# Kernel tuning notes

Measured on AMD Instinct MI355X. Metric: run time of the kernel, lower is better.

Reference implementation:

```python
import jax, jax.numpy as jnp
import numpy as np

B, S, F_IN, H, P2 = 64, 64, 2048, 512, 20  # batch, seq_len, input_size, hidden, 2*num_prototype


def setup_inputs() -> dict:
    key = jax.random.key(0)
    ks = jax.random.split(key, 16)
    sc = 0.02
    inp = {
        "v_feat": jax.random.normal(ks[0], (B, S, F_IN), jnp.float32),
        "category": jax.random.randint(ks[1], (B,), 0, 3, jnp.int64),
        "W_enc": jax.random.normal(ks[2], (F_IN, H), jnp.float32) * sc,
        "b_enc": jnp.zeros((H,), jnp.float32),
        # gate order along last axis: input, forget, output, memory(g)
        "Wx": jax.random.normal(ks[3], (H, 4 * H), jnp.float32) * sc,
        "bx": jnp.zeros((4 * H,), jnp.float32),
        "Wh": jax.random.normal(ks[4], (H, 4 * H), jnp.float32) * sc,
        "bh": jnp.zeros((4 * H,), jnp.float32),
        "cat_emb": jax.random.normal(ks[5], (3, H), jnp.float32) * sc,
        "W_dec": jax.random.normal(ks[6], (H, 1), jnp.float32) * sc,
        "b_dec": jnp.zeros((1,), jnp.float32),
        "prototype": jax.random.uniform(ks[7], (P2, F_IN), jnp.float32),
        "W_dd": jax.random.normal(ks[8], (P2 * S, 1), jnp.float32) * sc,
        "b_dd": jnp.zeros((1,), jnp.float32),
        "W_gate": jax.random.normal(ks[9], (F_IN, 1), jnp.float32) * sc,
        "b_gate": jnp.zeros((1,), jnp.float32),
    }
    return inp


def _forward(v_feat, category, W_enc, b_enc, Wx, bx, Wh, bh, cat_emb,
             W_dec, b_dec, prototype, W_dd, b_dd, W_gate, b_gate):
    batch, seq, feat = v_feat.shape
    # encoder + category fusion
    fuse = jax.nn.relu(jnp.einsum('bsf,fh->bsh', v_feat, W_enc) + b_enc)
    fuse = fuse + cat_emb[category][:, None, :]

    # fused-gate LSTM over time (note: original cell has NO tanh on cell in h = o*c)
    x_gates = jnp.einsum('bsh,hg->sbg', fuse, Wx) + (bx + bh)  # precompute input GEMM

    def step(carry, xg):
        h, c = carry
        gates = xg + h @ Wh
        i, f, o, g = jnp.split(gates, 4, axis=-1)
        i, f, o = jax.nn.sigmoid(i), jax.nn.sigmoid(f), jax.nn.sigmoid(o)
        g = jnp.tanh(g)
        c = f * c + i * g
        h = o * c
        return (h, c), None

    h0 = jnp.zeros((batch, Wh.shape[0]), fuse.dtype)
    (h, c), _ = jax.lax.scan(step, (h0, h0), x_gates)

    # dropout p=0.5 omitted (deterministic eval reference)
    output = jax.nn.sigmoid(h @ W_dec + b_dec)  # [B,1]

    # prototype distances: [B,S,2P]
    diff = v_feat[:, :, None, :] - prototype[None, None, :, :]
    dist = jnp.sum(diff * diff, axis=-1)
    dist_feat = jnp.log((dist + 1.0) / (dist + 1e-8))
    dist_pred = jax.nn.sigmoid(dist_feat.reshape(batch, -1) @ W_dd + b_dd)
    gate = jax.nn.sigmoid(jnp.mean(v_feat, axis=1) @ W_gate + b_gate)
    return output * gate + dist_pred * (1.0 - gate)


def reference(v_feat, category, W_enc, b_enc, Wx, bx, Wh, bh, cat_emb,
              W_dec, b_dec, prototype, W_dd, b_dd, W_gate, b_gate):
    return _forward(v_feat, category, W_enc, b_enc, Wx, bx, Wh, bh, cat_emb,
                    W_dec, b_dec, prototype, W_dd, b_dd, W_gate, b_gate)
```

## Files before the change

### kernel.cpp

```cpp
#include <hip/hip_runtime.h>
#include <cstdint>
#include <cstddef>


typedef __attribute__((ext_vector_type(8))) short short8;
typedef __attribute__((ext_vector_type(4))) float f32x4;
typedef unsigned long long ull;

__device__ __forceinline__ ushort f2bf(float x) {
    uint32_t u = __float_as_uint(x);
    return (ushort)((u + 0x7FFF + ((u >> 16) & 1)) >> 16);
}
__device__ __forceinline__ float bf2f(ushort u) {
    return __uint_as_float(((uint32_t)u) << 16);
}
__device__ __forceinline__ float sigm(float x) { return 1.f / (1.f + expf(-x)); }
__device__ __forceinline__ float tanh_fast(float x) { return 2.f / (1.f + expf(-2.f * x)) - 1.f; }

__global__ __launch_bounds__(256) void k_prep(
    const float* __restrict__ v_feat, const float* __restrict__ proto,
    const float* __restrict__ bx, const float* __restrict__ bh,
    const float* __restrict__ W_enc, const float* __restrict__ Wx,
    const float* __restrict__ Wh, const float* __restrict__ W_gate,
    ushort* __restrict__ v_bf16, ushort* __restrict__ proto_bf,
    float* __restrict__ bxh, ushort* __restrict__ Wenc_t,
    ushort* __restrict__ Wx_t, ushort* __restrict__ Whr,
    float* __restrict__ n2, float* __restrict__ gpart, float* __restrict__ p2,
    ushort* __restrict__ hbuf, int* __restrict__ flags, int* __restrict__ dd_done)
{
    __shared__ float ts[32][33];
    const int blk = blockIdx.x;
    const int tid = threadIdx.x;

    if (blk < 8192) {
        int i = blk * 256 + tid;
        float4 v = ((const float4*)v_feat)[i];
        ushort4 o;
        o.x = f2bf(v.x); o.y = f2bf(v.y); o.z = f2bf(v.z); o.w = f2bf(v.w);
        ((ushort4*)v_bf16)[i] = o;
    } else if (blk < 8232) {
        int i = (blk - 8192) * 256 + tid;
        float4 v = ((const float4*)proto)[i];
        ushort4 o;
        o.x = f2bf(v.x); o.y = f2bf(v.y); o.z = f2bf(v.z); o.w = f2bf(v.w);
        ((ushort4*)proto_bf)[i] = o;
    } else if (blk < 8244) {
        int row = 20 + (blk - 8232);
        ushort4 z = {0, 0, 0, 0};
        ((ushort4*)(proto_bf + (size_t)row * 2048))[tid * 2] = z;
        ((ushort4*)(proto_bf + (size_t)row * 2048))[tid * 2 + 1] = z;
    } else if (blk < 8252) {
        int n = (blk - 8244) * 256 + tid;
        int np = ((n & 511) << 2) | (n >> 9);
        bxh[np] = bx[n] + bh[n];
    } else if (blk < 11324) {
        const float* in;
        ushort* outp;
        int R, C, remap, t;
        if (blk < 9276)       { in = W_enc; outp = Wenc_t; R = 2048; C = 512;  remap = 0; t = blk - 8252; }
        else if (blk < 10300) { in = Wx;    outp = Wx_t;   R = 512;  C = 2048; remap = 1; t = blk - 9276; }
        else                  { in = Wh;    outp = Whr;    R = 512;  C = 2048; remap = 1; t = blk - 10300; }
        int tpr = C / 32;
        int cx = t % tpr, cy = t / tpr;
        int r0 = cy * 32, c0 = cx * 32;
        int rr = tid >> 3, cc = (tid & 7) * 4;
        float4 v = *(const float4*)(in + (size_t)(r0 + rr) * C + c0 + cc);
        ts[rr][cc + 0] = v.x; ts[rr][cc + 1] = v.y; ts[rr][cc + 2] = v.z; ts[rr][cc + 3] = v.w;
        __syncthreads();
        ushort4 o;
        o.x = f2bf(ts[cc + 0][rr]);
        o.y = f2bf(ts[cc + 1][rr]);
        o.z = f2bf(ts[cc + 2][rr]);
        o.w = f2bf(ts[cc + 3][rr]);
        int n = c0 + rr;
        int np = remap ? (((n & 511) << 2) | (n >> 9)) : n;
        *(ushort4*)(outp + (size_t)np * R + r0 + cc) = o;
    } else if (blk < 12348) {
        const int lane = tid & 63, w = tid >> 6;
        const int bs = (blk - 11324) * 4 + w;
        const float* vr = v_feat + (size_t)bs * 2048;
        float a = 0.f, g = 0.f;
#pragma unroll
        for (int i = 0; i < 8; ++i) {
            float4 x = ((const float4*)vr)[i * 64 + lane];
            float4 wg = ((const float4*)W_gate)[i * 64 + lane];
            a += x.x * x.x + x.y * x.y + x.z * x.z + x.w * x.w;
            g += x.x * wg.x + x.y * wg.y + x.z * wg.z + x.w * wg.w;
        }
#pragma unroll
        for (int o = 32; o > 0; o >>= 1) { a += __shfl_down(a, o); g += __shfl_down(g, o); }
        if (lane == 0) {
            n2[bs] = a;
            gpart[bs] = g;
        }
    } else if (blk == 12348) {
        const int lane = tid & 63, w = tid >> 6;
        for (int p = w; p < 20; p += 4) {
            const float* pr = proto + (size_t)p * 2048;
            float a = 0.f;
#pragma unroll
            for (int i = 0; i < 8; ++i) {
                float4 x = ((const float4*)pr)[i * 64 + lane];
                a += x.x * x.x + x.y * x.y + x.z * x.z + x.w * x.w;
            }
#pragma unroll
            for (int o = 32; o > 0; o >>= 1) a += __shfl_down(a, o);
            if (lane == 0) p2[p] = a;
        }
        if (tid == 0) *dd_done = 0;
    } else if (blk < 12381) {
        ((ull*)hbuf)[(blk - 12349) * 256 + tid] = 0ULL;
    } else {
        for (int i = tid; i < 2048; i += 256) flags[i] = 0;
    }
}

__global__ __launch_bounds__(256) void k_mid(
    const ushort* __restrict__ A, const ushort* __restrict__ Bt,
    const float* __restrict__ bias0,
    const float* __restrict__ cat_emb, const int* __restrict__ category,
    ushort* __restrict__ C,
    const ushort* __restrict__ proto_bf, float* __restrict__ dots)
{
    __shared__ ushort As[64][40];
    __shared__ ushort Bs[128][40];
    const int tid = threadIdx.x;
    const int lane = tid & 63, w = tid >> 6;
    const int quad = lane >> 4, l16 = lane & 15;
    const int blk = blockIdx.x;

    if (blk >= 256) {
        const int r0 = (blk - 256) * 64 + w * 16;
        f32x4 acc[2] = {};
        const ushort* arow = A + (size_t)(r0 + l16) * 2048 + quad * 8;
        const ushort* b0p = proto_bf + (size_t)l16 * 2048 + quad * 8;
        const ushort* b1p = proto_bf + (size_t)(16 + l16) * 2048 + quad * 8;
#pragma unroll 8
        for (int kk = 0; kk < 64; ++kk) {
            short8 af = *(const short8*)(arow + kk * 32);
            short8 bf0 = *(const short8*)(b0p + kk * 32);
            short8 bf1 = *(const short8*)(b1p + kk * 32);
            acc[0] = __builtin_amdgcn_mfma_f32_16x16x32_bf16(af, bf0, acc[0], 0, 0, 0);
            acc[1] = __builtin_amdgcn_mfma_f32_16x16x32_bf16(af, bf1, acc[1], 0, 0, 0);
        }
#pragma unroll
        for (int t = 0; t < 2; ++t)
#pragma unroll
            for (int r = 0; r < 4; ++r)
                dots[(size_t)(r0 + quad * 4 + r) * 32 + t * 16 + l16] = acc[t][r];
        return;
    }

    const int m0 = (blk >> 2) * 64, n0 = (blk & 3) * 128;
    const int wm = (w & 1) * 32, wn = (w >> 1) * 64;
    const int K = 2048;

    f32x4 acc[2][4] = {};
    const int lr = tid >> 2;
    const int lc = (tid & 3) * 8;

    for (int k0 = 0; k0 < K; k0 += 32) {
        uint4 a0 = *(const uint4*)(A + (size_t)(m0 + lr) * K + k0 + lc);
        uint4 b0 = *(const uint4*)(Bt + (size_t)(n0 + lr) * K + k0 + lc);
        uint4 b1 = *(const uint4*)(Bt + (size_t)(n0 + 64 + lr) * K + k0 + lc);
        __syncthreads();
        *(uint4*)&As[lr][lc] = a0;
        *(uint4*)&Bs[lr][lc] = b0;
        *(uint4*)&Bs[64 + lr][lc] = b1;
        __syncthreads();
        short8 af[2], bf[4];
#pragma unroll
        for (int i = 0; i < 2; ++i) af[i] = *(const short8*)&As[wm + i * 16 + l16][quad * 8];
#pragma unroll
        for (int j = 0; j < 4; ++j) bf[j] = *(const short8*)&Bs[wn + j * 16 + l16][quad * 8];
#pragma unroll
        for (int i = 0; i < 2; ++i)
#pragma unroll
            for (int j = 0; j < 4; ++j)
                acc[i][j] = __builtin_amdgcn_mfma_f32_16x16x32_bf16(af[i], bf[j], acc[i][j], 0, 0, 0);
    }

#pragma unroll
    for (int i = 0; i < 2; ++i) {
        int mbase = m0 + wm + i * 16 + quad * 4;
#pragma unroll
        for (int r = 0; r < 4; ++r) {
            int m = mbase + r;
            const float* ce = cat_emb + category[m >> 6] * 512;
#pragma unroll
            for (int j = 0; j < 4; ++j) {
                int n = n0 + wn + j * 16 + l16;
                float v = fmaxf(acc[i][j][r] + bias0[n], 0.f) + ce[n];
                C[(size_t)m * 512 + n] = f2bf(v);
            }
        }
    }
}

__global__ __launch_bounds__(256) void k_gemm_mfma(
    const ushort* __restrict__ A, const ushort* __restrict__ Bt,
    int M, int N, int K,
    const float* __restrict__ bias0,
    ushort* __restrict__ C)
{
    __shared__ ushort As[128][40];
    __shared__ ushort Bs[128][40];
    const int tid = threadIdx.x;
    const int lane = tid & 63, w = tid >> 6;
    const int quad = lane >> 4, l16 = lane & 15;
    const int m0 = blockIdx.y * 128, n0 = blockIdx.x * 128;
    const int wm = (w & 1) * 64, wn = (w >> 1) * 64;

    f32x4 acc[4][4] = {};
    const int lr = tid >> 2;
    const int lc = (tid & 3) * 8;

    for (int k0 = 0; k0 < K; k0 += 32) {
        uint4 a0 = *(const uint4*)(A + (size_t)(m0 + lr) * K + k0 + lc);
        uint4 a1 = *(const uint4*)(A + (size_t)(m0 + 64 + lr) * K + k0 + lc);
        uint4 b0 = *(const uint4*)(Bt + (size_t)(n0 + lr) * K + k0 + lc);
        uint4 b1 = *(const uint4*)(Bt + (size_t)(n0 + 64 + lr) * K + k0 + lc);
        __syncthreads();
        *(uint4*)&As[lr][lc] = a0;
        *(uint4*)&As[64 + lr][lc] = a1;
        *(uint4*)&Bs[lr][lc] = b0;
        *(uint4*)&Bs[64 + lr][lc] = b1;
        __syncthreads();
        short8 af[4], bf[4];
#pragma unroll
        for (int i = 0; i < 4; ++i) af[i] = *(const short8*)&As[wm + i * 16 + l16][quad * 8];
#pragma unroll
        for (int j = 0; j < 4; ++j) bf[j] = *(const short8*)&Bs[wn + j * 16 + l16][quad * 8];
#pragma unroll
        for (int i = 0; i < 4; ++i)
#pragma unroll
            for (int j = 0; j < 4; ++j)
                acc[i][j] = __builtin_amdgcn_mfma_f32_16x16x32_bf16(af[i], bf[j], acc[i][j], 0, 0, 0);
    }

    float bb[4];
#pragma unroll
    for (int j = 0; j < 4; ++j) bb[j] = bias0[n0 + wn + j * 16 + l16];
#pragma unroll
    for (int i = 0; i < 4; ++i) {
        int mbase = m0 + wm + i * 16 + quad * 4;
#pragma unroll
        for (int r = 0; r < 4; ++r) {
            int m = mbase + r;
            int s = m & 63, b = m >> 6;
            ushort* crow = C + ((size_t)(s * 64 + b)) * 2048;
#pragma unroll
            for (int j = 0; j < 4; ++j)
                crow[n0 + wn + j * 16 + l16] = f2bf(acc[i][j][r] + bb[j]);
        }
    }
}

__global__ __launch_bounds__(512, 2) void k_lstm_persist(
    const ushort* __restrict__ xg,
    const ushort* __restrict__ Whr,
    ushort* __restrict__ hbuf,
    int* __restrict__ flags,
    const float* __restrict__ W_dec, const float* __restrict__ b_dec,
    const float* __restrict__ b_dd, const float* __restrict__ b_gate,
    const float* __restrict__ dots, const float* __restrict__ n2,
    const float* __restrict__ p2, const float* __restrict__ W_dd,
    const float* __restrict__ gpart,
    float* __restrict__ dd_logit, float* __restrict__ g_logit,
    int* __restrict__ dd_done,
    float* __restrict__ out)
{
    __shared__ __align__(16) ushort hin_s[16 * 520];
    __shared__ __align__(16) ushort hstage[512];
    __shared__ float fred[8][64];

    const int tid = threadIdx.x;
    const int lane = tid & 63, wv = tid >> 6;
    const int quad = lane >> 4, l16 = lane & 15;
    const int bn = blockIdx.x;

    if (bn >= 64) {
        const int b = bn - 64;
        if (tid < 64) {
            float gp = gpart[b * 64 + tid];
#pragma unroll
            for (int o = 32; o > 0; o >>= 1) gp += __shfl_down(gp, o);
            if (tid == 0)
                __hip_atomic_store(&g_logit[b], gp, __ATOMIC_RELAXED, __HIP_MEMORY_SCOPE_AGENT);
        }
        float acc = 0.f;
        for (int u = tid; u < 1280; u += 512) {
            int s = u / 20, p = u - s * 20;
            int bs = b * 64 + s;
            float d = n2[bs] - 2.f * dots[(size_t)bs * 32 + p] + p2[p];
            acc += logf((d + 1.0f) / (d + 1e-8f)) * W_dd[s * 20 + p];
        }
#pragma unroll
        for (int o = 32; o > 0; o >>= 1) acc += __shfl_down(acc, o);
        if (lane == 0) fred[wv][0] = acc;
        __syncthreads();
        if (tid == 0) {
            float t = 0.f;
#pragma unroll
            for (int p = 0; p < 8; ++p) t += fred[p][0];
            __hip_atomic_store(&dd_logit[b], t, __ATOMIC_RELAXED, __HIP_MEMORY_SCOPE_AGENT);
            __hip_atomic_fetch_add(dd_done, 1, __ATOMIC_RELEASE, __HIP_MEMORY_SCOPE_AGENT);
        }
        return;
    }

    const int i = bn & 15;
    const int j = bn >> 4;
    const int uloc = wv * 4 + quad;

    short8 wfrag[16];
#pragma unroll
    for (int kc = 0; kc < 16; ++kc)
        wfrag[kc] = *(const short8*)(Whr +
            (size_t)(i * 128 + wv * 16 + l16) * 512 + kc * 32 + quad * 8);

    float c = 0.f;

    for (int s = 0; s < 64; ++s) {
        const ushort* xp = xg + (size_t)(s * 64 + j * 16 + l16) * 2048
                              + i * 128 + wv * 16 + quad * 4;
        ushort4 xa = *(const ushort4*)xp;

        if (s > 0) {
            if (tid < 16) {
                const int* f = flags + (j * 16 + tid) * 32;
                while (__hip_atomic_load(f, __ATOMIC_RELAXED,
                                         __HIP_MEMORY_SCOPE_AGENT) < s) {}
            }
            __builtin_amdgcn_s_barrier();
            asm volatile("" ::: "memory");
        }
        const ushort* hin = hbuf + (size_t)s * 32768 + j * 8192;
        ushort* hout = hbuf + (size_t)(s + 1) * 32768 + j * 8192;

        {
            int r0 = wv * 2;
            __builtin_amdgcn_global_load_lds(
                (const __attribute__((address_space(1))) void*)(hin + (size_t)r0 * 512 + lane * 8),
                (__attribute__((address_space(3))) void*)(hin_s + r0 * 520),
                16, 0, 0);
            __builtin_amdgcn_global_load_lds(
                (const __attribute__((address_space(1))) void*)(hin + (size_t)(r0 + 1) * 512 + lane * 8),
                (__attribute__((address_space(3))) void*)(hin_s + (r0 + 1) * 520),
                16, 0, 0);
        }
        asm volatile("s_waitcnt vmcnt(0)" ::: "memory");
        __builtin_amdgcn_s_barrier();
        asm volatile("" ::: "memory");

        f32x4 aA = {bf2f(xa.x), bf2f(xa.y), bf2f(xa.z), bf2f(xa.w)};
        f32x4 aB = {};
#pragma unroll
        for (int kc = 0; kc < 16; kc += 2) {
            short8 h0 = *(const short8*)(hin_s + l16 * 520 + kc * 32 + quad * 8);
            short8 h1 = *(const short8*)(hin_s + l16 * 520 + (kc + 1) * 32 + quad * 8);
            aA = __builtin_amdgcn_mfma_f32_16x16x32_bf16(wfrag[kc], h0, aA, 0, 0, 0);
            aB = __builtin_amdgcn_mfma_f32_16x16x32_bf16(wfrag[kc + 1], h1, aB, 0, 0, 0);
        }

        float gi = sigm(aA[0] + aB[0]);
        float gf = sigm(aA[1] + aB[1]);
        float go = sigm(aA[2] + aB[2]);
        float gg = tanh_fast(aA[3] + aB[3]);
        c = gf * c + gi * gg;
        hstage[l16 * 32 + uloc] = f2bf(go * c);

        asm volatile("s_waitcnt lgkmcnt(0)" ::: "memory");
        __builtin_amdgcn_s_barrier();
        asm volatile("" ::: "memory");

        if (tid < 128) {
            int r = tid >> 3, ch = tid & 7;
            __hip_atomic_store((ull*)(hout + (size_t)r * 512 + i * 32) + ch,
                               ((const ull*)hstage)[tid],
                               __ATOMIC_RELAXED, __HIP_MEMORY_SCOPE_AGENT);
        }
        __syncthreads();
        if (tid == 0)
            __hip_atomic_store(&flags[bn * 32], s + 1, __ATOMIC_RELAXED,
                               __HIP_MEMORY_SCOPE_AGENT);
    }

    if (bn == 0) {
        if (tid < 64) {
            while (__hip_atomic_load(&flags[tid * 32], __ATOMIC_RELAXED,
                                     __HIP_MEMORY_SCOPE_AGENT) < 64) {}
        }
        __syncthreads();
        asm volatile("" ::: "memory");
        const ushort* hb64 = hbuf + (size_t)64 * 32768;
        int b = tid & 63, part = tid >> 6;
        const ushort* row = hb64 + (size_t)(b >> 4) * 8192 + (b & 15) * 512;
        float acc = 0.f;
#pragma unroll
        for (int g8 = 0; g8 < 8; ++g8) {
            const ushort* hp = row + part * 64 + g8 * 8;
            const float* wd = W_dec + part * 64 + g8 * 8;
#pragma unroll
            for (int half = 0; half < 2; ++half) {
                ull u = *(const ull*)(hp + half * 4);
                acc += bf2f((ushort)u) * wd[half * 4]
                     + bf2f((ushort)(u >> 16)) * wd[half * 4 + 1]
                     + bf2f((ushort)(u >> 32)) * wd[half * 4 + 2]
                     + bf2f((ushort)(u >> 48)) * wd[half * 4 + 3];
            }
        }
        fred[part][b] = acc;
        __syncthreads();
        if (tid == 0) {
            while (__hip_atomic_load(dd_done, __ATOMIC_RELAXED,
                                     __HIP_MEMORY_SCOPE_AGENT) < 64) {}
        }
        __syncthreads();
        asm volatile("" ::: "memory");
        if (tid < 64) {
            float a = 0.f;
#pragma unroll
            for (int p = 0; p < 8; ++p) a += fred[p][tid];
            float gl = __hip_atomic_load(&g_logit[tid], __ATOMIC_RELAXED,
                                         __HIP_MEMORY_SCOPE_AGENT);
            float dl = __hip_atomic_load(&dd_logit[tid], __ATOMIC_RELAXED,
                                         __HIP_MEMORY_SCOPE_AGENT);
            float output = sigm(a + b_dec[0]);
            float gate   = sigm(gl * (1.0f / 64.f) + b_gate[0]);
            float ddp    = sigm(dl + b_dd[0]);
            out[tid] = output * gate + ddp * (1.f - gate);
        }
    }
}

extern "C" void kernel_launch(void* const* d_in, const int* in_sizes, int n_in,
                              void* d_out, int out_size, void* d_ws, size_t ws_size,
                              hipStream_t stream) {
    const float* v_feat   = (const float*)d_in[0];
    const int*   category = (const int*)d_in[1];
    const float* W_enc    = (const float*)d_in[2];
    const float* b_enc    = (const float*)d_in[3];
    const float* Wx       = (const float*)d_in[4];
    const float* bx       = (const float*)d_in[5];
    const float* Wh       = (const float*)d_in[6];
    const float* bh       = (const float*)d_in[7];
    const float* cat_emb  = (const float*)d_in[8];
    const float* W_dec    = (const float*)d_in[9];
    const float* b_dec    = (const float*)d_in[10];
    const float* proto    = (const float*)d_in[11];
    const float* W_dd     = (const float*)d_in[12];
    const float* b_dd     = (const float*)d_in[13];
    const float* W_gate   = (const float*)d_in[14];
    const float* b_gate   = (const float*)d_in[15];
    float* out = (float*)d_out;

    char* ws = (char*)d_ws;
    ushort* xg       = (ushort*)(ws + 0);
    ushort* v_bf16   = (ushort*)(ws + 0);
    ushort* fuse     = (ushort*)(ws + 16777216);
    ushort* Whr      = (ushort*)(ws + 20971520);
    ushort* Wenc_t   = (ushort*)(ws + 23068672);
    ushort* Wx_t     = (ushort*)(ws + 25165824);
    ushort* proto_bf = (ushort*)(ws + 27262976);
    float*  dots     = (float*)(ws + 27394048);
    float*  n2       = (float*)(ws + 27918336);
    float*  gpart    = (float*)(ws + 27934720);
    float*  p2       = (float*)(ws + 27951104);
    int*    dd_done  = (int*)(ws + 27951232);
    float*  bxh      = (float*)(ws + 27951616);
    int*    flags    = (int*)(ws + 27959808);
    float*  dd_logit = (float*)(ws + 27967744);
    float*  g_logit  = (float*)(ws + 27968000);
    ushort* hbuf     = (ushort*)(ws + 27968256);

    k_prep<<<12382, 256, 0, stream>>>(v_feat, proto, bx, bh, W_enc, Wx, Wh, W_gate,
                                      v_bf16, proto_bf, bxh, Wenc_t, Wx_t, Whr,
                                      n2, gpart, p2, hbuf, flags, dd_done);

    k_mid<<<320, 256, 0, stream>>>(v_bf16, Wenc_t, b_enc, cat_emb, category,
                                   fuse, proto_bf, dots);

    k_gemm_mfma<<<dim3(16, 32), 256, 0, stream>>>(fuse, Wx_t, 4096, 2048, 512,
                                                  bxh, xg);

    k_lstm_persist<<<128, 512, 0, stream>>>(xg, Whr, hbuf, flags,
                                            W_dec, b_dec, b_dd, b_gate,
                                            dots, n2, p2, W_dd, gpart,
                                            dd_logit, g_logit, dd_done, out);
}
```

Before: 235.6 us.

## Interleave two batch groups per LSTM block to hide inter-block step latency

```diff
diff --git a/kernel.cpp b/kernel.cpp
--- a/kernel.cpp
+++ b/kernel.cpp
@@ -271,7 +271,8 @@
     float* __restrict__ out)
 {
     __shared__ __align__(16) ushort hin_s[16 * 520];
-    __shared__ __align__(16) ushort hstage[512];
+    __shared__ __align__(16) ushort hstageA[512];
+    __shared__ __align__(16) ushort hstageB[512];
     __shared__ float fred[8][64];
 
     const int tid = threadIdx.x;
@@ -279,8 +280,8 @@
     const int quad = lane >> 4, l16 = lane & 15;
     const int bn = blockIdx.x;
 
-    if (bn >= 64) {
-        const int b = bn - 64;
+    if (bn >= 32) {
+        const int b = bn - 32;
         if (tid < 64) {
             float gp = gpart[b * 64 + tid];
 #pragma unroll
@@ -310,7 +311,8 @@
     }
 
     const int i = bn & 15;
-    const int j = bn >> 4;
+    const int t = bn >> 4;
+    const int gA = t * 2, gB = t * 2 + 1;
     const int uloc = wv * 4 + quad;
 
     short8 wfrag[16];
@@ -319,25 +321,19 @@
         wfrag[kc] = *(const short8*)(Whr +
             (size_t)(i * 128 + wv * 16 + l16) * 512 + kc * 32 + quad * 8);
 
-    float c = 0.f;
-
-    for (int s = 0; s < 64; ++s) {
-        const ushort* xp = xg + (size_t)(s * 64 + j * 16 + l16) * 2048
-                              + i * 128 + wv * 16 + quad * 4;
-        ushort4 xa = *(const ushort4*)xp;
-
-        if (s > 0) {
-            if (tid < 16) {
-                const int* f = flags + (j * 16 + tid) * 32;
-                while (__hip_atomic_load(f, __ATOMIC_RELAXED,
-                                         __HIP_MEMORY_SCOPE_AGENT) < s) {}
-            }
-            __builtin_amdgcn_s_barrier();
-            asm volatile("" ::: "memory");
-        }
-        const ushort* hin = hbuf + (size_t)s * 32768 + j * 8192;
-        ushort* hout = hbuf + (size_t)(s + 1) * 32768 + j * 8192;
-
+    const int fAidx = (gA * 16 + i) * 32;
+    const int fBidx = (gB * 16 + i) * 32;
+
+    float cA = 0.f, cB = 0.f;
+
+    auto phase = [&](int g, float& c, ushort* hstage_l, const ushort4& xa,
+                     int s, bool doPoll, bool setFlag, int flagIdx, int flagVal) {
+        if (doPoll && tid < 16) {
+            const int* f = flags + (g * 16 + tid) * 32;
+            while (__hip_atomic_load(f, __ATOMIC_RELAXED,
+                                     __HIP_MEMORY_SCOPE_AGENT) < s) {}
+        }
+        const ushort* hin = hbuf + (size_t)s * 32768 + g * 8192;
         {
             int r0 = wv * 2;
             __builtin_amdgcn_global_load_lds(
@@ -352,6 +348,9 @@
         asm volatile("s_waitcnt vmcnt(0)" ::: "memory");
         __builtin_amdgcn_s_barrier();
         asm volatile("" ::: "memory");
+        if (setFlag && tid == 0)
+            __hip_atomic_store(&flags[flagIdx], flagVal, __ATOMIC_RELAXED,
+                               __HIP_MEMORY_SCOPE_AGENT);
 
         f32x4 aA = {bf2f(xa.x), bf2f(xa.y), bf2f(xa.z), bf2f(xa.w)};
         f32x4 aB = {};
@@ -368,23 +367,35 @@
         float go = sigm(aA[2] + aB[2]);
         float gg = tanh_fast(aA[3] + aB[3]);
         c = gf * c + gi * gg;
-        hstage[l16 * 32 + uloc] = f2bf(go * c);
+        hstage_l[l16 * 32 + uloc] = f2bf(go * c);
 
         asm volatile("s_waitcnt lgkmcnt(0)" ::: "memory");
         __builtin_amdgcn_s_barrier();
         asm volatile("" ::: "memory");
 
         if (tid < 128) {
+            ushort* hout = hbuf + (size_t)(s + 1) * 32768 + g * 8192;
             int r = tid >> 3, ch = tid & 7;
             __hip_atomic_store((ull*)(hout + (size_t)r * 512 + i * 32) + ch,
-                               ((const ull*)hstage)[tid],
+                               ((const ull*)hstage_l)[tid],
                                __ATOMIC_RELAXED, __HIP_MEMORY_SCOPE_AGENT);
         }
-        __syncthreads();
-        if (tid == 0)
-            __hip_atomic_store(&flags[bn * 32], s + 1, __ATOMIC_RELAXED,
-                               __HIP_MEMORY_SCOPE_AGENT);
-    }
+    };
+
+    for (int s = 0; s < 64; ++s) {
+        ushort4 xaA = *(const ushort4*)(xg + (size_t)(s * 64 + gA * 16 + l16) * 2048
+                                           + i * 128 + wv * 16 + quad * 4);
+        ushort4 xaB = *(const ushort4*)(xg + (size_t)(s * 64 + gB * 16 + l16) * 2048
+                                           + i * 128 + wv * 16 + quad * 4);
+        phase(gA, cA, hstageA, xaA, s, s > 0, s > 0, fBidx, s);
+        phase(gB, cB, hstageB, xaB, s, s > 0, true, fAidx, s + 1);
+    }
+    asm volatile("s_waitcnt vmcnt(0)" ::: "memory");
+    __builtin_amdgcn_s_barrier();
+    asm volatile("" ::: "memory");
+    if (tid == 0)
+        __hip_atomic_store(&flags[fBidx], 64, __ATOMIC_RELAXED,
+                           __HIP_MEMORY_SCOPE_AGENT);
 
     if (bn == 0) {
         if (tid < 64) {
@@ -484,8 +495,8 @@
     k_gemm_mfma<<<dim3(16, 32), 256, 0, stream>>>(fuse, Wx_t, 4096, 2048, 512,
                                                   bxh, xg);
 
-    k_lstm_persist<<<128, 512, 0, stream>>>(xg, Whr, hbuf, flags,
-                                            W_dec, b_dec, b_dd, b_gate,
-                                            dots, n2, p2, W_dd, gpart,
-                                            dd_logit, g_logit, dd_done, out);
-}
+    k_lstm_persist<<<96, 512, 0, stream>>>(xg, Whr, hbuf, flags,
+                                           W_dec, b_dec, b_dd, b_gate,
+                                           dots, n2, p2, W_dd, gpart,
+                                           dd_logit, g_logit, dd_done, out);
+}
```

New measurement: 329.0 us. 1.4x slower.

## Fuse input-gate GEMM into persistent LSTM kernel with per-tile ready flags

Applied to the files above, without the earlier changes.

```diff
diff --git a/kernel.cpp b/kernel.cpp
--- a/kernel.cpp
+++ b/kernel.cpp
@@ -26,40 +26,60 @@
     float* __restrict__ bxh, ushort* __restrict__ Wenc_t,
     ushort* __restrict__ Wx_t, ushort* __restrict__ Whr,
     float* __restrict__ n2, float* __restrict__ gpart, float* __restrict__ p2,
-    ushort* __restrict__ hbuf, int* __restrict__ flags, int* __restrict__ dd_done)
+    ushort* __restrict__ hbuf, int* __restrict__ flags, int* __restrict__ dd_done,
+    int* __restrict__ xgf)
 {
     __shared__ float ts[32][33];
     const int blk = blockIdx.x;
     const int tid = threadIdx.x;
 
-    if (blk < 8192) {
-        int i = blk * 256 + tid;
-        float4 v = ((const float4*)v_feat)[i];
-        ushort4 o;
-        o.x = f2bf(v.x); o.y = f2bf(v.y); o.z = f2bf(v.z); o.w = f2bf(v.w);
-        ((ushort4*)v_bf16)[i] = o;
-    } else if (blk < 8232) {
-        int i = (blk - 8192) * 256 + tid;
+    if (blk < 4096) {
+        const int bs = blk;
+        const float* vr = v_feat + (size_t)bs * 2048;
+        float4 x0 = ((const float4*)vr)[tid];
+        float4 x1 = ((const float4*)vr)[tid + 256];
+        float4 w0 = ((const float4*)W_gate)[tid];
+        float4 w1 = ((const float4*)W_gate)[tid + 256];
+        ushort4 o0, o1;
+        o0.x = f2bf(x0.x); o0.y = f2bf(x0.y); o0.z = f2bf(x0.z); o0.w = f2bf(x0.w);
+        o1.x = f2bf(x1.x); o1.y = f2bf(x1.y); o1.z = f2bf(x1.z); o1.w = f2bf(x1.w);
+        ((ushort4*)v_bf16)[(size_t)bs * 512 + tid] = o0;
+        ((ushort4*)v_bf16)[(size_t)bs * 512 + tid + 256] = o1;
+        float a = x0.x * x0.x + x0.y * x0.y + x0.z * x0.z + x0.w * x0.w
+                + x1.x * x1.x + x1.y * x1.y + x1.z * x1.z + x1.w * x1.w;
+        float g = x0.x * w0.x + x0.y * w0.y + x0.z * w0.z + x0.w * w0.w
+                + x1.x * w1.x + x1.y * w1.y + x1.z * w1.z + x1.w * w1.w;
+        const int lane = tid & 63, w = tid >> 6;
+#pragma unroll
+        for (int o = 32; o > 0; o >>= 1) { a += __shfl_down(a, o); g += __shfl_down(g, o); }
+        if (lane == 0) { ts[0][w] = a; ts[1][w] = g; }
+        __syncthreads();
+        if (tid == 0) {
+            n2[bs]    = ts[0][0] + ts[0][1] + ts[0][2] + ts[0][3];
+            gpart[bs] = ts[1][0] + ts[1][1] + ts[1][2] + ts[1][3];
+        }
+    } else if (blk < 4136) {
+        int i = (blk - 4096) * 256 + tid;
         float4 v = ((const float4*)proto)[i];
         ushort4 o;
         o.x = f2bf(v.x); o.y = f2bf(v.y); o.z = f2bf(v.z); o.w = f2bf(v.w);
         ((ushort4*)proto_bf)[i] = o;
-    } else if (blk < 8244) {
-        int row = 20 + (blk - 8232);
+    } else if (blk < 4148) {
+        int row = 20 + (blk - 4136);
         ushort4 z = {0, 0, 0, 0};
         ((ushort4*)(proto_bf + (size_t)row * 2048))[tid * 2] = z;
         ((ushort4*)(proto_bf + (size_t)row * 2048))[tid * 2 + 1] = z;
-    } else if (blk < 8252) {
-        int n = (blk - 8244) * 256 + tid;
+    } else if (blk < 4156) {
+        int n = (blk - 4148) * 256 + tid;
         int np = ((n & 511) << 2) | (n >> 9);
         bxh[np] = bx[n] + bh[n];
-    } else if (blk < 11324) {
+    } else if (blk < 7228) {
         const float* in;
         ushort* outp;
         int R, C, remap, t;
-        if (blk < 9276)       { in = W_enc; outp = Wenc_t; R = 2048; C = 512;  remap = 0; t = blk - 8252; }
-        else if (blk < 10300) { in = Wx;    outp = Wx_t;   R = 512;  C = 2048; remap = 1; t = blk - 9276; }
-        else                  { in = Wh;    outp = Whr;    R = 512;  C = 2048; remap = 1; t = blk - 10300; }
+        if (blk < 5180)      { in = W_enc; outp = Wenc_t; R = 2048; C = 512;  remap = 0; t = blk - 4156; }
+        else if (blk < 6204) { in = Wx;    outp = Wx_t;   R = 512;  C = 2048; remap = 1; t = blk - 5180; }
+        else                 { in = Wh;    outp = Whr;    R = 512;  C = 2048; remap = 1; t = blk - 6204; }
         int tpr = C / 32;
         int cx = t % tpr, cy = t / tpr;
         int r0 = cy * 32, c0 = cx * 32;
@@ -75,25 +95,7 @@
         int n = c0 + rr;
         int np = remap ? (((n & 511) << 2) | (n >> 9)) : n;
         *(ushort4*)(outp + (size_t)np * R + r0 + cc) = o;
-    } else if (blk < 12348) {
-        const int lane = tid & 63, w = tid >> 6;
-        const int bs = (blk - 11324) * 4 + w;
-        const float* vr = v_feat + (size_t)bs * 2048;
-        float a = 0.f, g = 0.f;
-#pragma unroll
-        for (int i = 0; i < 8; ++i) {
-            float4 x = ((const float4*)vr)[i * 64 + lane];
-            float4 wg = ((const float4*)W_gate)[i * 64 + lane];
-            a += x.x * x.x + x.y * x.y + x.z * x.z + x.w * x.w;
-            g += x.x * wg.x + x.y * wg.y + x.z * wg.z + x.w * wg.w;
-        }
-#pragma unroll
-        for (int o = 32; o > 0; o >>= 1) { a += __shfl_down(a, o); g += __shfl_down(g, o); }
-        if (lane == 0) {
-            n2[bs] = a;
-            gpart[bs] = g;
-        }
-    } else if (blk == 12348) {
+    } else if (blk == 7228) {
         const int lane = tid & 63, w = tid >> 6;
         for (int p = w; p < 20; p += 4) {
             const float* pr = proto + (size_t)p * 2048;
@@ -108,10 +110,11 @@
             if (lane == 0) p2[p] = a;
         }
         if (tid == 0) *dd_done = 0;
-    } else if (blk < 12381) {
-        ((ull*)hbuf)[(blk - 12349) * 256 + tid] = 0ULL;
+    } else if (blk < 7261) {
+        ((ull*)hbuf)[(blk - 7229) * 256 + tid] = 0ULL;
     } else {
         for (int i = tid; i < 2048; i += 256) flags[i] = 0;
+        for (int i = tid; i < 512; i += 256) xgf[i] = 0;
     }
 }
 
@@ -197,67 +200,12 @@
     }
 }
 
-__global__ __launch_bounds__(256) void k_gemm_mfma(
-    const ushort* __restrict__ A, const ushort* __restrict__ Bt,
-    int M, int N, int K,
-    const float* __restrict__ bias0,
-    ushort* __restrict__ C)
-{
-    __shared__ ushort As[128][40];
-    __shared__ ushort Bs[128][40];
-    const int tid = threadIdx.x;
-    const int lane = tid & 63, w = tid >> 6;
-    const int quad = lane >> 4, l16 = lane & 15;
-    const int m0 = blockIdx.y * 128, n0 = blockIdx.x * 128;
-    const int wm = (w & 1) * 64, wn = (w >> 1) * 64;
-
-    f32x4 acc[4][4] = {};
-    const int lr = tid >> 2;
-    const int lc = (tid & 3) * 8;
-
-    for (int k0 = 0; k0 < K; k0 += 32) {
-        uint4 a0 = *(const uint4*)(A + (size_t)(m0 + lr) * K + k0 + lc);
-        uint4 a1 = *(const uint4*)(A + (size_t)(m0 + 64 + lr) * K + k0 + lc);
-        uint4 b0 = *(const uint4*)(Bt + (size_t)(n0 + lr) * K + k0 + lc);
-        uint4 b1 = *(const uint4*)(Bt + (size_t)(n0 + 64 + lr) * K + k0 + lc);
-        __syncthreads();
-        *(uint4*)&As[lr][lc] = a0;
-        *(uint4*)&As[64 + lr][lc] = a1;
-        *(uint4*)&Bs[lr][lc] = b0;
-        *(uint4*)&Bs[64 + lr][lc] = b1;
-        __syncthreads();
-        short8 af[4], bf[4];
-#pragma unroll
-        for (int i = 0; i < 4; ++i) af[i] = *(const short8*)&As[wm + i * 16 + l16][quad * 8];
-#pragma unroll
-        for (int j = 0; j < 4; ++j) bf[j] = *(const short8*)&Bs[wn + j * 16 + l16][quad * 8];
-#pragma unroll
-        for (int i = 0; i < 4; ++i)
-#pragma unroll
-            for (int j = 0; j < 4; ++j)
-                acc[i][j] = __builtin_amdgcn_mfma_f32_16x16x32_bf16(af[i], bf[j], acc[i][j], 0, 0, 0);
-    }
-
-    float bb[4];
-#pragma unroll
-    for (int j = 0; j < 4; ++j) bb[j] = bias0[n0 + wn + j * 16 + l16];
-#pragma unroll
-    for (int i = 0; i < 4; ++i) {
-        int mbase = m0 + wm + i * 16 + quad * 4;
-#pragma unroll
-        for (int r = 0; r < 4; ++r) {
-            int m = mbase + r;
-            int s = m & 63, b = m >> 6;
-            ushort* crow = C + ((size_t)(s * 64 + b)) * 2048;
-#pragma unroll
-            for (int j = 0; j < 4; ++j)
-                crow[n0 + wn + j * 16 + l16] = f2bf(acc[i][j][r] + bb[j]);
-        }
-    }
-}
-
 __global__ __launch_bounds__(512, 2) void k_lstm_persist(
-    const ushort* __restrict__ xg,
+    ushort* __restrict__ xg,
+    const ushort* __restrict__ fuse,
+    const ushort* __restrict__ Wx_t,
+    const float* __restrict__ bxh,
+    int* __restrict__ xgf,
     const ushort* __restrict__ Whr,
     ushort* __restrict__ hbuf,
     int* __restrict__ flags,
@@ -273,14 +221,16 @@
     __shared__ __align__(16) ushort hin_s[16 * 520];
     __shared__ __align__(16) ushort hstage[512];
     __shared__ float fred[8][64];
+    __shared__ __align__(16) ushort As[128][40];
+    __shared__ __align__(16) ushort Bs[128][40];
 
     const int tid = threadIdx.x;
     const int lane = tid & 63, wv = tid >> 6;
     const int quad = lane >> 4, l16 = lane & 15;
     const int bn = blockIdx.x;
 
-    if (bn >= 64) {
-        const int b = bn - 64;
+    if (bn >= 320) {
+        const int b = bn - 320;
         if (tid < 64) {
             float gp = gpart[b * 64 + tid];
 #pragma unroll
@@ -309,6 +259,63 @@
         return;
     }
 
+    if (bn >= 64) {
+        const int g = bn - 64;
+        const int nc = g & 15;
+        const int n0 = nc * 128;
+        const int lrA = tid >> 2;
+        const int lcA = (tid & 3) * 8;
+        const int w8 = tid >> 6;
+        const int wm8 = (w8 & 3) * 32, wn8 = (w8 >> 2) * 64;
+
+#pragma unroll
+        for (int ph = 0; ph < 2; ++ph) {
+            const int mt = (ph ? 16 : 0) + (g >> 4);
+            const int m0 = mt * 128;
+            f32x4 acc[2][4] = {};
+            for (int k0 = 0; k0 < 512; k0 += 32) {
+                int ma = m0 + lrA;
+                int fr = ((ma & 63) << 6) | (ma >> 6);
+                uint4 a0 = *(const uint4*)(fuse + (size_t)fr * 512 + k0 + lcA);
+                uint4 b0 = *(const uint4*)(Wx_t + (size_t)(n0 + lrA) * 512 + k0 + lcA);
+                __syncthreads();
+                *(uint4*)&As[lrA][lcA] = a0;
+                *(uint4*)&Bs[lrA][lcA] = b0;
+                __syncthreads();
+                short8 af[2], bf[4];
+#pragma unroll
+                for (int i = 0; i < 2; ++i) af[i] = *(const short8*)&As[wm8 + i * 16 + l16][quad * 8];
+#pragma unroll
+                for (int j = 0; j < 4; ++j) bf[j] = *(const short8*)&Bs[wn8 + j * 16 + l16][quad * 8];
+#pragma unroll
+                for (int i = 0; i < 2; ++i)
+#pragma unroll
+                    for (int j = 0; j < 4; ++j)
+                        acc[i][j] = __builtin_amdgcn_mfma_f32_16x16x32_bf16(af[i], bf[j], acc[i][j], 0, 0, 0);
+            }
+            float bb[4];
+#pragma unroll
+            for (int j = 0; j < 4; ++j) bb[j] = bxh[n0 + wn8 + j * 16 + l16];
+#pragma unroll
+            for (int i = 0; i < 2; ++i) {
+                int mbase = m0 + wm8 + i * 16 + quad * 4;
+#pragma unroll
+                for (int r = 0; r < 4; ++r) {
+                    ushort* crow = xg + (size_t)(mbase + r) * 2048;
+#pragma unroll
+                    for (int j = 0; j < 4; ++j)
+                        crow[n0 + wn8 + j * 16 + l16] = f2bf(acc[i][j][r] + bb[j]);
+                }
+            }
+            asm volatile("s_waitcnt vmcnt(0)" ::: "memory");
+            __syncthreads();
+            if (tid == 0)
+                __hip_atomic_store(&xgf[mt * 16 + nc], 1, __ATOMIC_RELAXED,
+                                   __HIP_MEMORY_SCOPE_AGENT);
+        }
+        return;
+    }
+
     const int i = bn & 15;
     const int j = bn >> 4;
     const int uloc = wv * 4 + quad;
@@ -322,19 +329,31 @@
     float c = 0.f;
 
     for (int s = 0; s < 64; ++s) {
-        const ushort* xp = xg + (size_t)(s * 64 + j * 16 + l16) * 2048
-                              + i * 128 + wv * 16 + quad * 4;
-        ushort4 xa = *(const ushort4*)xp;
-
         if (s > 0) {
             if (tid < 16) {
                 const int* f = flags + (j * 16 + tid) * 32;
                 while (__hip_atomic_load(f, __ATOMIC_RELAXED,
                                          __HIP_MEMORY_SCOPE_AGENT) < s) {}
+            } else if (tid == 16) {
+                const int xi = (s >> 1) * 16 + i;
+                while (__hip_atomic_load(&xgf[xi], __ATOMIC_RELAXED,
+                                         __HIP_MEMORY_SCOPE_AGENT) == 0) {}
             }
             __builtin_amdgcn_s_barrier();
             asm volatile("" ::: "memory");
-        }
+        } else {
+            if (tid == 0) {
+                while (__hip_atomic_load(&xgf[i], __ATOMIC_RELAXED,
+                                         __HIP_MEMORY_SCOPE_AGENT) == 0) {}
+            }
+            __builtin_amdgcn_s_barrier();
+            asm volatile("" ::: "memory");
+        }
+
+        const ushort* xp = xg + (size_t)(s * 64 + j * 16 + l16) * 2048
+                              + i * 128 + wv * 16 + quad * 4;
+        ushort4 xa = *(const ushort4*)xp;
+
         const ushort* hin = hbuf + (size_t)s * 32768 + j * 8192;
         ushort* hout = hbuf + (size_t)(s + 1) * 32768 + j * 8192;
 
@@ -473,18 +492,17 @@
     float*  dd_logit = (float*)(ws + 27967744);
     float*  g_logit  = (float*)(ws + 27968000);
     ushort* hbuf     = (ushort*)(ws + 27968256);
-
-    k_prep<<<12382, 256, 0, stream>>>(v_feat, proto, bx, bh, W_enc, Wx, Wh, W_gate,
-                                      v_bf16, proto_bf, bxh, Wenc_t, Wx_t, Whr,
-                                      n2, gpart, p2, hbuf, flags, dd_done);
+    int*    xgf      = (int*)(ws + 32228096);
+
+    k_prep<<<7262, 256, 0, stream>>>(v_feat, proto, bx, bh, W_enc, Wx, Wh, W_gate,
+                                     v_bf16, proto_bf, bxh, Wenc_t, Wx_t, Whr,
+                                     n2, gpart, p2, hbuf, flags, dd_done, xgf);
 
     k_mid<<<320, 256, 0, stream>>>(v_bf16, Wenc_t, b_enc, cat_emb, category,
                                    fuse, proto_bf, dots);
 
-    k_gemm_mfma<<<dim3(16, 32), 256, 0, stream>>>(fuse, Wx_t, 4096, 2048, 512,
-                                                  bxh, xg);
-
-    k_lstm_persist<<<128, 512, 0, stream>>>(xg, Whr, hbuf, flags,
+    k_lstm_persist<<<384, 512, 0, stream>>>(xg, fuse, Wx_t, bxh, xgf,
+                                            Whr, hbuf, flags,
                                             W_dec, b_dec, b_dd, b_gate,
                                             dots, n2, p2, W_dd, gpart,
                                             dd_logit, g_logit, dd_done, out);
```

New measurement: 231.9 us. About the same (-1.5%).
